# Performance work log

Measured on AMD Instinct MI355X. Metric: run time of the kernel, lower is better.

Reference implementation:

```python
import jax, jax.numpy as jnp
import numpy as np

N = 8192
D = 2048      # input_dim
DH = 1024     # input_dim // r
DO = 1024     # output_dim

def setup_inputs() -> dict:
    key = jax.random.key(0)
    ks = jax.random.split(key, 11)
    s_in = 1.0 / np.sqrt(D)
    s_h = 1.0 / np.sqrt(DH)
    return {
        "O0": jax.random.normal(ks[0], (N, D), dtype=jnp.float32),
        "Ww": jax.random.uniform(ks[1], (DH, D), jnp.float32, -s_in, s_in),
        "Wb": jax.random.uniform(ks[2], (DH,), jnp.float32, -s_in, s_in),
        "Uw": jax.random.uniform(ks[3], (DH, D), jnp.float32, -s_in, s_in),
        "Ub": jax.random.uniform(ks[4], (DH,), jnp.float32, -s_in, s_in),
        "Hw": jax.random.uniform(ks[5], (DH, D), jnp.float32, -s_in, s_in),
        "Hb": jax.random.uniform(ks[6], (DH,), jnp.float32, -s_in, s_in),
        "fc0w": jax.random.uniform(ks[7], (D, DH), jnp.float32, -s_h, s_h),
        "fc0b": jax.random.uniform(ks[8], (D,), jnp.float32, -s_h, s_h),
        "fc1w": jax.random.uniform(ks[9], (DO, D), jnp.float32, -s_in, s_in),
        "fc1b": jax.random.uniform(ks[10], (DO,), jnp.float32, -s_in, s_in),
    }

def reference(O0, Ww, Wb, Uw, Ub, Hw, Hb, fc0w, fc0b, fc1w, fc1b):
    q = O0 @ Ww.T + Wb              # [N, DH]
    k = O0 @ Uw.T + Ub              # [N, DH]
    v = O0 @ Hw.T + Hb              # [N, DH]
    scores = q @ k.T                # [N, N], unscaled as in the original
    R1 = jax.nn.softmax(scores, axis=1)
    ctx = R1 @ v                    # [N, DH]
    O1 = O0 + (ctx @ fc0w.T + fc0b) # residual, [N, D]
    O2 = O1 @ fc1w.T + fc1b         # [N, DO]
    return (O1, O2)
```

## Files before the change

kernel.cpp:

```cpp
#include <hip/hip_runtime.h>
#include <cstdint>
#include <cstddef>

typedef _Float16 f16;
typedef _Float16 f16x8 __attribute__((ext_vector_type(8)));
typedef _Float16 f16x4 __attribute__((ext_vector_type(4)));
typedef float    f32x4 __attribute__((ext_vector_type(4)));

#define BM 128
#define BN 128
#define BK 64

__global__ __launch_bounds__(256) void cvt_f32_f16(const float* __restrict__ in,
                                                   f16* __restrict__ out, int n) {
  int i = (blockIdx.x * 256 + threadIdx.x) * 4;
  if (i < n) {
    float4 v = *(const float4*)(in + i);
    f16x4 h; h[0] = (f16)v.x; h[1] = (f16)v.y; h[2] = (f16)v.z; h[3] = (f16)v.w;
    *(f16x4*)(out + i) = h;
  }
}

__global__ __launch_bounds__(256) void transpose_f16(const f16* __restrict__ in,
                                                     int ldi,
                                                     f16* __restrict__ out,
                                                     int R, int C) {
  __shared__ f16 tile[64][65];
  const int r0 = blockIdx.y * 64, c0 = blockIdx.x * 64;
  const int t = threadIdx.x;
#pragma unroll
  for (int p = 0; p < 2; p++) {
    int s = t + p * 256;
    int r = s >> 3, q = s & 7;
    f16x8 v = *(const f16x8*)(in + (size_t)(r0 + r) * ldi + c0 + q * 8);
#pragma unroll
    for (int e = 0; e < 8; e++) tile[r][q * 8 + e] = v[e];
  }
  __syncthreads();
#pragma unroll
  for (int p = 0; p < 2; p++) {
    int s = t + p * 256;
    int r = s >> 3, q = s & 7;
    f16x8 v;
#pragma unroll
    for (int e = 0; e < 8; e++) v[e] = tile[q * 8 + e][r];
    *(f16x8*)(out + (size_t)(c0 + r) * R + r0 + q * 8) = v;
  }
}

template <int MODE>
__global__ __launch_bounds__(256) void gemm_bt(
    const f16* __restrict__ A, const f16* __restrict__ B,
    int M, int N, int K, int lda, int ldb,
    const float* __restrict__ bias,
    f16* __restrict__ outH, int ldo,
    float* __restrict__ statsM, float* __restrict__ statsS, int sld,
    const float* __restrict__ alphaT,
    const float* __restrict__ resid, int ldr,
    float* __restrict__ outF, int ldof) {
  __shared__ f16 lA[BM * BK];
  __shared__ f16 lB[BN * BK];
  const int t = threadIdx.x;
  const int m0 = blockIdx.y * BM, n0 = blockIdx.x * BN;
  const int wave = t >> 6, lane = t & 63;
  const int wr = wave >> 1, wc = wave & 1;
  const int quad = lane >> 4, l16 = lane & 15;

  const int rc = lane >> 3;
  const int kcs = (lane & 7) ^ rc;
  const uint32_t offA = (uint32_t)(rc * lda + kcs * 8) * 2u;
  const uint32_t offB = (uint32_t)(rc * ldb + kcs * 8) * 2u;
  const char* bAp = (const char*)(A + (size_t)m0 * lda);
  const char* bBp = (const char*)(B + (size_t)n0 * ldb);
  const int wq = __builtin_amdgcn_readfirstlane(wave * 4);

  f32x4 acc[4][4];
#pragma unroll
  for (int i = 0; i < 4; i++)
#pragma unroll
    for (int j = 0; j < 4; j++)
#pragma unroll
      for (int e = 0; e < 4; e++) acc[i][j][e] = 0.0f;

  const int nk = K / BK;
  for (int kt = 0; kt < nk; ++kt) {
    float al[4];
    if constexpr (MODE == 2) {
      const float* ap = alphaT + (size_t)kt * M + m0 + wr * 64 + l16;
      al[0] = ap[0]; al[1] = ap[16]; al[2] = ap[32]; al[3] = ap[48];
    }
    const size_t kb = (size_t)(kt * BK) * 2;
#pragma unroll
    for (int j = 0; j < 4; j++) {
      const int c = wq + j;
      __builtin_amdgcn_global_load_lds(
          (const __attribute__((address_space(1))) void*)
              (bAp + ((size_t)(c * 8) * lda * 2 + kb) + offA),
          (__attribute__((address_space(3))) void*)(lA + c * 512), 16, 0, 0);
      __builtin_amdgcn_global_load_lds(
          (const __attribute__((address_space(1))) void*)
              (bBp + ((size_t)(c * 8) * ldb * 2 + kb) + offB),
          (__attribute__((address_space(3))) void*)(lB + c * 512), 16, 0, 0);
    }
    __syncthreads();

    f16x8 af[2][4], bf[2][4];
#pragma unroll
    for (int h = 0; h < 2; h++) {
      const int p = ((h * 4 + quad) ^ (l16 & 7)) * 8;
#pragma unroll
      for (int i = 0; i < 4; i++)
        af[h][i] = *(const f16x8*)(lA + (wr * 64 + i * 16 + l16) * 64 + p);
#pragma unroll
      for (int j = 0; j < 4; j++)
        bf[h][j] = *(const f16x8*)(lB + (wc * 64 + j * 16 + l16) * 64 + p);
    }
    if constexpr (MODE == 2) {
#pragma unroll
      for (int i = 0; i < 4; i++) {
        const f16 ah = (f16)al[i];
        af[0][i] = af[0][i] * ah;
        af[1][i] = af[1][i] * ah;
      }
    }
#pragma unroll
    for (int h = 0; h < 2; h++)
#pragma unroll
      for (int i = 0; i < 4; i++)
#pragma unroll
        for (int j = 0; j < 4; j++)
          acc[i][j] = __builtin_amdgcn_mfma_f32_16x16x32_f16(af[h][i], bf[h][j],
                                                             acc[i][j], 0, 0, 0);
    __syncthreads();
  }

  const int mrow = m0 + wr * 64;
  const int ncol = n0 + wc * 64;
  float bv[4];
  if constexpr (MODE == 0 || MODE == 3 || MODE == 4) {
#pragma unroll
    for (int j = 0; j < 4; j++) bv[j] = bias[ncol + j * 16 + l16];
  }
#pragma unroll
  for (int fi = 0; fi < 4; fi++) {
#pragma unroll
    for (int i = 0; i < 4; i++) {
      const int gr = mrow + fi * 16 + quad * 4 + i;
      if constexpr (MODE == 1) {
        float mx = fmaxf(fmaxf(acc[fi][0][i], acc[fi][1][i]),
                         fmaxf(acc[fi][2][i], acc[fi][3][i]));
        mx = fmaxf(mx, __shfl_xor(mx, 1));
        mx = fmaxf(mx, __shfl_xor(mx, 2));
        mx = fmaxf(mx, __shfl_xor(mx, 4));
        mx = fmaxf(mx, __shfl_xor(mx, 8));
        float e0 = __expf(acc[fi][0][i] - mx);
        float e1 = __expf(acc[fi][1][i] - mx);
        float e2 = __expf(acc[fi][2][i] - mx);
        float e3 = __expf(acc[fi][3][i] - mx);
        float sm = (e0 + e1) + (e2 + e3);
        sm += __shfl_xor(sm, 1);
        sm += __shfl_xor(sm, 2);
        sm += __shfl_xor(sm, 4);
        sm += __shfl_xor(sm, 8);
        if (l16 == 0) {
          statsM[(size_t)gr * sld + (blockIdx.x * 2 + wc)] = mx;
          statsS[(size_t)gr * sld + (blockIdx.x * 2 + wc)] = sm;
        }
        f16* rp = outH + (size_t)gr * ldo + ncol + l16;
        rp[0]  = (f16)e0;
        rp[16] = (f16)e1;
        rp[32] = (f16)e2;
        rp[48] = (f16)e3;
      } else if constexpr (MODE == 0) {
        f16* rp = outH + (size_t)gr * ldo + ncol + l16;
        rp[0]  = (f16)(acc[fi][0][i] + bv[0]);
        rp[16] = (f16)(acc[fi][1][i] + bv[1]);
        rp[32] = (f16)(acc[fi][2][i] + bv[2]);
        rp[48] = (f16)(acc[fi][3][i] + bv[3]);
      } else if constexpr (MODE == 2) {
        f16* rp = outH + (size_t)gr * ldo + ncol + l16;
        rp[0]  = (f16)acc[fi][0][i];
        rp[16] = (f16)acc[fi][1][i];
        rp[32] = (f16)acc[fi][2][i];
        rp[48] = (f16)acc[fi][3][i];
      } else if constexpr (MODE == 3) {
        float* rf = outF + (size_t)gr * ldof + ncol + l16;
        const float* rr = resid + (size_t)gr * ldr + ncol + l16;
        f16* rh = outH + (size_t)gr * ldo + ncol + l16;
        float o0 = acc[fi][0][i] + bv[0] + rr[0];
        float o1 = acc[fi][1][i] + bv[1] + rr[16];
        float o2 = acc[fi][2][i] + bv[2] + rr[32];
        float o3 = acc[fi][3][i] + bv[3] + rr[48];
        rf[0] = o0; rf[16] = o1; rf[32] = o2; rf[48] = o3;
        rh[0] = (f16)o0; rh[16] = (f16)o1; rh[32] = (f16)o2; rh[48] = (f16)o3;
      } else {
        float* rf = outF + (size_t)gr * ldof + ncol + l16;
        rf[0]  = acc[fi][0][i] + bv[0];
        rf[16] = acc[fi][1][i] + bv[1];
        rf[32] = acc[fi][2][i] + bv[2];
        rf[48] = acc[fi][3][i] + bv[3];
      }
    }
  }
}

__global__ __launch_bounds__(256) void alpha_from_stats(
    const float* __restrict__ sM, const float* __restrict__ sS,
    float* __restrict__ aT, int rows) {
  __shared__ float alph[128][65];
  const int t = threadIdx.x;
  const int r = t >> 2, j = t & 3;
  const int row = blockIdx.x * 64 + r;
  const float* pm = sM + (size_t)row * 128 + j * 32;
  const float* ps = sS + (size_t)row * 128 + j * 32;
  float mv[32];
  float mx = -1e30f;
#pragma unroll
  for (int c = 0; c < 32; c++) { mv[c] = pm[c]; mx = fmaxf(mx, mv[c]); }
  mx = fmaxf(mx, __shfl_xor(mx, 1));
  mx = fmaxf(mx, __shfl_xor(mx, 2));
  float ev[32];
  float sum = 0.0f;
#pragma unroll
  for (int c = 0; c < 32; c++) {
    ev[c] = __expf(mv[c] - mx);
    sum += ev[c] * ps[c];
  }
  sum += __shfl_xor(sum, 1);
  sum += __shfl_xor(sum, 2);
  const float rl = 1.0f / sum;
#pragma unroll
  for (int c = 0; c < 32; c++) alph[j * 32 + c][r] = ev[c] * rl;
  __syncthreads();
  const int wid = t >> 6, rr = t & 63;
#pragma unroll
  for (int c = 0; c < 32; c++) {
    const int tg = c * 4 + wid;
    aT[(size_t)tg * rows + blockIdx.x * 64 + rr] = alph[tg][rr];
  }
}

extern "C" void kernel_launch(void* const* d_in, const int* in_sizes, int n_in,
                              void* d_out, int out_size, void* d_ws, size_t ws_size,
                              hipStream_t stream) {
  const float* O0   = (const float*)d_in[0];
  const float* Ww   = (const float*)d_in[1];
  const float* Wb   = (const float*)d_in[2];
  const float* Uw   = (const float*)d_in[3];
  const float* Ub   = (const float*)d_in[4];
  const float* Hw   = (const float*)d_in[5];
  const float* Hb   = (const float*)d_in[6];
  const float* fc0w = (const float*)d_in[7];
  const float* fc0b = (const float*)d_in[8];
  const float* fc1w = (const float*)d_in[9];
  const float* fc1b = (const float*)d_in[10];

  const int N = 8192, D = 2048, DH = 1024, DO = 1024;
  const int NQKV = 3 * DH;

  char* w = (char*)d_ws;
  f16* Wwh   = (f16*)w; w += (size_t)DH * D * 2;
  f16* Uwh   = (f16*)w; w += (size_t)DH * D * 2;
  f16* Hwh   = (f16*)w; w += (size_t)DH * D * 2;
  f16* fc0wh = (f16*)w; w += (size_t)D * DH * 2;
  f16* fc1wh = (f16*)w; w += (size_t)DO * D * 2;
  float* aT  = (float*)w; w += (size_t)128 * N * 4;
  char* un = w; w += (size_t)N * DH * 2;
  float* statsM = (float*)un;
  float* statsS = statsM + (size_t)N * 128;
  f16* ctxh = (f16*)un;
  float* biasC = (float*)w; w += (size_t)NQKV * 4;
  w = (char*)(((uintptr_t)w + 255) & ~(uintptr_t)255);
  f16* Sb = (f16*)w;

  f16* oh   = (f16*)d_out;
  f16* qkv  = oh;
  f16* qh   = qkv;
  f16* kh   = qkv + DH;
  f16* vh   = qkv + 2 * DH;
  f16* O0h  = oh + (size_t)N * NQKV;
  f16* vT   = O0h + (size_t)N * D;
  f16* O1h  = Sb;

  {
    int n = DH * D;
    int grid = n / 1024;
    cvt_f32_f16<<<grid, 256, 0, stream>>>(Ww, Wwh, n);
    cvt_f32_f16<<<grid, 256, 0, stream>>>(Uw, Uwh, n);
    cvt_f32_f16<<<grid, 256, 0, stream>>>(Hw, Hwh, n);
    cvt_f32_f16<<<grid, 256, 0, stream>>>(fc0w, fc0wh, n);
    cvt_f32_f16<<<grid, 256, 0, stream>>>(fc1w, fc1wh, n);
    cvt_f32_f16<<<(N * D) / 1024, 256, 0, stream>>>(O0, O0h, N * D);
    hipMemcpyAsync(biasC,          Wb, DH * 4, hipMemcpyDeviceToDevice, stream);
    hipMemcpyAsync(biasC + DH,     Ub, DH * 4, hipMemcpyDeviceToDevice, stream);
    hipMemcpyAsync(biasC + 2 * DH, Hb, DH * 4, hipMemcpyDeviceToDevice, stream);
  }

  gemm_bt<0><<<dim3(NQKV / BN, N / BM), 256, 0, stream>>>(
      O0h, Wwh, N, NQKV, D, D, D, biasC,
      qkv, NQKV, nullptr, nullptr, 0, nullptr, nullptr, 0, nullptr, 0);

  transpose_f16<<<dim3(DH / 64, N / 64), 256, 0, stream>>>(vh, NQKV, vT, N, DH);

  gemm_bt<1><<<dim3(N / BN, N / BM), 256, 0, stream>>>(
      qh, kh, N, N, DH, NQKV, NQKV, nullptr, Sb, N,
      statsM, statsS, 128, nullptr, nullptr, 0, nullptr, 0);

  alpha_from_stats<<<N / 64, 256, 0, stream>>>(statsM, statsS, aT, N);

  gemm_bt<2><<<dim3(DH / BN, N / BM), 256, 0, stream>>>(
      Sb, vT, N, DH, N, N, N, nullptr, ctxh, DH,
      nullptr, nullptr, 0, aT, nullptr, 0, nullptr, 0);

  gemm_bt<3><<<dim3(D / BN, N / BM), 256, 0, stream>>>(
      ctxh, fc0wh, N, D, DH, DH, DH, fc0b, O1h, D,
      nullptr, nullptr, 0, nullptr, O0, D, (float*)d_out, D);

  gemm_bt<4><<<dim3(DO / BN, N / BM), 256, 0, stream>>>(
      O1h, fc1wh, N, DO, D, D, D, fc1b, nullptr, 0,
      nullptr, nullptr, 0, nullptr, nullptr, 0,
      (float*)d_out + (size_t)N * D, DO);
}
```

Before: 841.9 us.

## Replace 128x128 GEMM with double-buffered 256x256 ping-pong MFMA kernel

Swaps the single-buffered 128x128, 256-thread GEMM for a 256x256, 512-thread kernel. Its LDS stages are double-buffered, and global-to-LDS loads for the next k-tiles are interleaved with quarter-tile MFMA bursts. MFMA sections run at raised wave priority, and a block-index swizzle is added to improve L2 reuse. The aim is to raise arithmetic intensity and hide load latency behind compute. In exchange it uses about 130KB of LDS per block, and the narrow GEMMs (ctx and fc1) now launch only 128 workgroups, which may leave many CUs idle.

```diff
diff --git a/kernel.cpp b/kernel.cpp
--- a/kernel.cpp
+++ b/kernel.cpp
@@ -7,9 +7,7 @@
 typedef _Float16 f16x4 __attribute__((ext_vector_type(4)));
 typedef float    f32x4 __attribute__((ext_vector_type(4)));
 
-#define BM 128
-#define BN 128
-#define BK 64
+template <int V> struct IC { static constexpr int v = V; };
 
 __global__ __launch_bounds__(256) void cvt_f32_f16(const float* __restrict__ in,
                                                    f16* __restrict__ out, int n) {
@@ -49,7 +47,7 @@
 }
 
 template <int MODE>
-__global__ __launch_bounds__(256) void gemm_bt(
+__global__ __launch_bounds__(512, 2) void gemm256(
     const f16* __restrict__ A, const f16* __restrict__ B,
     int M, int N, int K, int lda, int ldb,
     const float* __restrict__ bias,
@@ -58,147 +56,233 @@
     const float* __restrict__ alphaT,
     const float* __restrict__ resid, int ldr,
     float* __restrict__ outF, int ldof) {
-  __shared__ f16 lA[BM * BK];
-  __shared__ f16 lB[BN * BK];
+  __shared__ f16 lA[2][2][128 * 64];
+  __shared__ f16 lB[2][2][128 * 64];
+  __shared__ float lAl[2][256];
+
   const int t = threadIdx.x;
-  const int m0 = blockIdx.y * BM, n0 = blockIdx.x * BN;
   const int wave = t >> 6, lane = t & 63;
-  const int wr = wave >> 1, wc = wave & 1;
+  const int wr = wave >> 2, wc = wave & 3;
   const int quad = lane >> 4, l16 = lane & 15;
-
   const int rc = lane >> 3;
   const int kcs = (lane & 7) ^ rc;
-  const uint32_t offA = (uint32_t)(rc * lda + kcs * 8) * 2u;
-  const uint32_t offB = (uint32_t)(rc * ldb + kcs * 8) * 2u;
-  const char* bAp = (const char*)(A + (size_t)m0 * lda);
-  const char* bBp = (const char*)(B + (size_t)n0 * ldb);
-  const int wq = __builtin_amdgcn_readfirstlane(wave * 4);
-
-  f32x4 acc[4][4];
-#pragma unroll
-  for (int i = 0; i < 4; i++)
-#pragma unroll
-    for (int j = 0; j < 4; j++)
-#pragma unroll
-      for (int e = 0; e < 4; e++) acc[i][j][e] = 0.0f;
-
-  const int nk = K / BK;
-  for (int kt = 0; kt < nk; ++kt) {
-    float al[4];
+
+  const int nwg = gridDim.x * gridDim.y;
+  const int bid = blockIdx.y * gridDim.x + blockIdx.x;
+  const int sb = (bid & 7) * (nwg >> 3) + (bid >> 3);
+  const int bx = sb % gridDim.x, by = sb / gridDim.x;
+  const int m0 = by * 256, n0 = bx * 256;
+  const int nk = K >> 6;
+
+  const f16* Abase = A + (size_t)m0 * lda;
+  const f16* Bbase = B + (size_t)n0 * ldb;
+
+  auto stageA = [&](int tau, int h) {
+    if (tau >= nk) return;
+    const f16* src = Abase + (size_t)(h * 128 + rc) * lda + tau * 64 + kcs * 8;
+    f16* dstu = &lA[tau & 1][h][0];
+#pragma unroll
+    for (int j = 0; j < 2; j++) {
+      const int sl = j * 8 + wave;
+      __builtin_amdgcn_global_load_lds(
+          (const __attribute__((address_space(1))) void*)(src + (size_t)sl * 8 * lda),
+          (__attribute__((address_space(3))) void*)(dstu + sl * 512), 16, 0, 0);
+    }
+  };
+  auto stageB = [&](int tau, int h) {
+    if (tau >= nk) return;
+    const f16* src = Bbase + (size_t)(h * 128 + rc) * ldb + tau * 64 + kcs * 8;
+    f16* dstu = &lB[tau & 1][h][0];
+#pragma unroll
+    for (int j = 0; j < 2; j++) {
+      const int sl = j * 8 + wave;
+      __builtin_amdgcn_global_load_lds(
+          (const __attribute__((address_space(1))) void*)(src + (size_t)sl * 8 * ldb),
+          (__attribute__((address_space(3))) void*)(dstu + sl * 512), 16, 0, 0);
+    }
+  };
+  auto stageAl = [&](int tau) {
     if constexpr (MODE == 2) {
-      const float* ap = alphaT + (size_t)kt * M + m0 + wr * 64 + l16;
-      al[0] = ap[0]; al[1] = ap[16]; al[2] = ap[32]; al[3] = ap[48];
-    }
-    const size_t kb = (size_t)(kt * BK) * 2;
-#pragma unroll
-    for (int j = 0; j < 4; j++) {
-      const int c = wq + j;
+      if (tau >= nk) return;
       __builtin_amdgcn_global_load_lds(
-          (const __attribute__((address_space(1))) void*)
-              (bAp + ((size_t)(c * 8) * lda * 2 + kb) + offA),
-          (__attribute__((address_space(3))) void*)(lA + c * 512), 16, 0, 0);
-      __builtin_amdgcn_global_load_lds(
-          (const __attribute__((address_space(1))) void*)
-              (bBp + ((size_t)(c * 8) * ldb * 2 + kb) + offB),
-          (__attribute__((address_space(3))) void*)(lB + c * 512), 16, 0, 0);
-    }
-    __syncthreads();
-
-    f16x8 af[2][4], bf[2][4];
-#pragma unroll
-    for (int h = 0; h < 2; h++) {
-      const int p = ((h * 4 + quad) ^ (l16 & 7)) * 8;
-#pragma unroll
-      for (int i = 0; i < 4; i++)
-        af[h][i] = *(const f16x8*)(lA + (wr * 64 + i * 16 + l16) * 64 + p);
-#pragma unroll
-      for (int j = 0; j < 4; j++)
-        bf[h][j] = *(const f16x8*)(lB + (wc * 64 + j * 16 + l16) * 64 + p);
-    }
-    if constexpr (MODE == 2) {
-#pragma unroll
-      for (int i = 0; i < 4; i++) {
-        const f16 ah = (f16)al[i];
-        af[0][i] = af[0][i] * ah;
-        af[1][i] = af[1][i] * ah;
+          (const __attribute__((address_space(1))) void*)(alphaT + (size_t)tau * M + m0 + lane * 4),
+          (__attribute__((address_space(3))) void*)(&lAl[tau & 1][0]), 16, 0, 0);
+    }
+  };
+
+  f32x4 acc[2][4][2][2];
+#pragma unroll
+  for (int mh = 0; mh < 2; mh++)
+#pragma unroll
+    for (int i = 0; i < 4; i++)
+#pragma unroll
+      for (int nh = 0; nh < 2; nh++)
+#pragma unroll
+        for (int j = 0; j < 2; j++)
+#pragma unroll
+          for (int e = 0; e < 4; e++) acc[mh][i][nh][j][e] = 0.0f;
+
+  f16x8 af[4][2];
+  f16x8 bf[2][2][2];
+
+  auto readA = [&](auto BUFC, auto MHC) {
+    constexpr int buf = decltype(BUFC)::v;
+    constexpr int mh = decltype(MHC)::v;
+#pragma unroll
+    for (int i = 0; i < 4; i++) {
+      const int r = i * 32 + wr * 16 + l16;
+#pragma unroll
+      for (int s = 0; s < 2; s++) {
+        const int p = ((s * 4 + quad) ^ (l16 & 7)) * 8;
+        af[i][s] = *(const f16x8*)(&lA[buf][mh][r * 64 + p]);
       }
-    }
-#pragma unroll
-    for (int h = 0; h < 2; h++)
-#pragma unroll
-      for (int i = 0; i < 4; i++)
-#pragma unroll
-        for (int j = 0; j < 4; j++)
-          acc[i][j] = __builtin_amdgcn_mfma_f32_16x16x32_f16(af[h][i], bf[h][j],
-                                                             acc[i][j], 0, 0, 0);
-    __syncthreads();
-  }
-
-  const int mrow = m0 + wr * 64;
-  const int ncol = n0 + wc * 64;
+      if constexpr (MODE == 2) {
+        const f16 ah = (f16)lAl[buf][mh * 128 + r];
+        af[i][0] = af[i][0] * ah;
+        af[i][1] = af[i][1] * ah;
+      }
+    }
+  };
+  auto readB = [&](auto BUFC, auto NHC) {
+    constexpr int buf = decltype(BUFC)::v;
+    constexpr int nh = decltype(NHC)::v;
+    const int hb = wc >> 1;
+#pragma unroll
+    for (int j = 0; j < 2; j++) {
+      const int r = (wc & 1) * 64 + nh * 32 + j * 16 + l16;
+#pragma unroll
+      for (int s = 0; s < 2; s++) {
+        const int p = ((s * 4 + quad) ^ (l16 & 7)) * 8;
+        bf[nh][j][s] = *(const f16x8*)(&lB[buf][hb][r * 64 + p]);
+      }
+    }
+  };
+  auto mfmaQ = [&](auto MHC, auto NHC) {
+    constexpr int mh = decltype(MHC)::v;
+    constexpr int nh = decltype(NHC)::v;
+    __builtin_amdgcn_s_setprio(1);
+#pragma unroll
+    for (int i = 0; i < 4; i++)
+#pragma unroll
+      for (int j = 0; j < 2; j++)
+#pragma unroll
+        for (int s = 0; s < 2; s++)
+          acc[mh][i][nh][j] = __builtin_amdgcn_mfma_f32_16x16x32_f16(
+              af[i][s], bf[nh][j][s], acc[mh][i][nh][j], 0, 0, 0);
+    __builtin_amdgcn_s_setprio(0);
+  };
+
+  auto tile4 = [&](auto BUFC, int tt, bool dr) {
+    readA(BUFC, IC<0>{});
+    readB(BUFC, IC<0>{});
+    stageA(tt + 1, 1);
+    stageAl(tt + 1);
+    __builtin_amdgcn_s_barrier();
+    asm volatile("s_waitcnt lgkmcnt(0)" ::: "memory");
+    mfmaQ(IC<0>{}, IC<0>{});
+    __builtin_amdgcn_s_barrier();
+    readB(BUFC, IC<1>{});
+    stageA(tt + 2, 0);
+    __builtin_amdgcn_s_barrier();
+    asm volatile("s_waitcnt lgkmcnt(0)" ::: "memory");
+    mfmaQ(IC<0>{}, IC<1>{});
+    __builtin_amdgcn_s_barrier();
+    readA(BUFC, IC<1>{});
+    stageB(tt + 2, 0);
+    __builtin_amdgcn_s_barrier();
+    asm volatile("s_waitcnt lgkmcnt(0)" ::: "memory");
+    mfmaQ(IC<1>{}, IC<1>{});
+    __builtin_amdgcn_s_barrier();
+    stageB(tt + 2, 1);
+    __builtin_amdgcn_s_barrier();
+    mfmaQ(IC<1>{}, IC<0>{});
+    if (dr) { asm volatile("s_waitcnt vmcnt(0)" ::: "memory"); }
+    else    { asm volatile("s_waitcnt vmcnt(6)" ::: "memory"); }
+    __builtin_amdgcn_s_barrier();
+  };
+
+  stageA(0, 0); stageB(0, 0); stageB(0, 1); stageA(0, 1);
+  stageAl(0);
+  stageA(1, 0); stageB(1, 0); stageB(1, 1);
+  asm volatile("s_waitcnt vmcnt(6)" ::: "memory");
+  __builtin_amdgcn_s_barrier();
+
+  for (int tt = 0; tt < nk; tt += 2) {
+    const bool dr = (tt + 2 >= nk);
+    tile4(IC<0>{}, tt, dr);
+    tile4(IC<1>{}, tt + 1, dr);
+  }
+
+  const int colb = n0 + wc * 64 + l16;
   float bv[4];
   if constexpr (MODE == 0 || MODE == 3 || MODE == 4) {
 #pragma unroll
-    for (int j = 0; j < 4; j++) bv[j] = bias[ncol + j * 16 + l16];
-  }
-#pragma unroll
-  for (int fi = 0; fi < 4; fi++) {
+    for (int c = 0; c < 4; c++) bv[c] = bias[colb + c * 16];
+  }
+#pragma unroll
+  for (int mh = 0; mh < 2; mh++) {
 #pragma unroll
     for (int i = 0; i < 4; i++) {
-      const int gr = mrow + fi * 16 + quad * 4 + i;
-      if constexpr (MODE == 1) {
-        float mx = fmaxf(fmaxf(acc[fi][0][i], acc[fi][1][i]),
-                         fmaxf(acc[fi][2][i], acc[fi][3][i]));
-        mx = fmaxf(mx, __shfl_xor(mx, 1));
-        mx = fmaxf(mx, __shfl_xor(mx, 2));
-        mx = fmaxf(mx, __shfl_xor(mx, 4));
-        mx = fmaxf(mx, __shfl_xor(mx, 8));
-        float e0 = __expf(acc[fi][0][i] - mx);
-        float e1 = __expf(acc[fi][1][i] - mx);
-        float e2 = __expf(acc[fi][2][i] - mx);
-        float e3 = __expf(acc[fi][3][i] - mx);
-        float sm = (e0 + e1) + (e2 + e3);
-        sm += __shfl_xor(sm, 1);
-        sm += __shfl_xor(sm, 2);
-        sm += __shfl_xor(sm, 4);
-        sm += __shfl_xor(sm, 8);
-        if (l16 == 0) {
-          statsM[(size_t)gr * sld + (blockIdx.x * 2 + wc)] = mx;
-          statsS[(size_t)gr * sld + (blockIdx.x * 2 + wc)] = sm;
+#pragma unroll
+      for (int e = 0; e < 4; e++) {
+        const int gr = m0 + mh * 128 + i * 32 + wr * 16 + quad * 4 + e;
+        const float v0 = acc[mh][i][0][0][e];
+        const float v1 = acc[mh][i][0][1][e];
+        const float v2 = acc[mh][i][1][0][e];
+        const float v3 = acc[mh][i][1][1][e];
+        if constexpr (MODE == 1) {
+          float mx = fmaxf(fmaxf(v0, v1), fmaxf(v2, v3));
+          mx = fmaxf(mx, __shfl_xor(mx, 1));
+          mx = fmaxf(mx, __shfl_xor(mx, 2));
+          mx = fmaxf(mx, __shfl_xor(mx, 4));
+          mx = fmaxf(mx, __shfl_xor(mx, 8));
+          float e0 = __expf(v0 - mx);
+          float e1 = __expf(v1 - mx);
+          float e2 = __expf(v2 - mx);
+          float e3 = __expf(v3 - mx);
+          float sm = (e0 + e1) + (e2 + e3);
+          sm += __shfl_xor(sm, 1);
+          sm += __shfl_xor(sm, 2);
+          sm += __shfl_xor(sm, 4);
+          sm += __shfl_xor(sm, 8);
+          if (l16 == 0) {
+            statsM[(size_t)gr * sld + (bx * 4 + wc)] = mx;
+            statsS[(size_t)gr * sld + (bx * 4 + wc)] = sm;
+          }
+          f16* rp = outH + (size_t)gr * ldo + colb;
+          rp[0]  = (f16)e0;
+          rp[16] = (f16)e1;
+          rp[32] = (f16)e2;
+          rp[48] = (f16)e3;
+        } else if constexpr (MODE == 0) {
+          f16* rp = outH + (size_t)gr * ldo + colb;
+          rp[0]  = (f16)(v0 + bv[0]);
+          rp[16] = (f16)(v1 + bv[1]);
+          rp[32] = (f16)(v2 + bv[2]);
+          rp[48] = (f16)(v3 + bv[3]);
+        } else if constexpr (MODE == 2) {
+          f16* rp = outH + (size_t)gr * ldo + colb;
+          rp[0]  = (f16)v0;
+          rp[16] = (f16)v1;
+          rp[32] = (f16)v2;
+          rp[48] = (f16)v3;
+        } else if constexpr (MODE == 3) {
+          float* rf = outF + (size_t)gr * ldof + colb;
+          const float* rr = resid + (size_t)gr * ldr + colb;
+          f16* rh = outH + (size_t)gr * ldo + colb;
+          float o0 = v0 + bv[0] + rr[0];
+          float o1 = v1 + bv[1] + rr[16];
+          float o2 = v2 + bv[2] + rr[32];
+          float o3 = v3 + bv[3] + rr[48];
+          rf[0] = o0; rf[16] = o1; rf[32] = o2; rf[48] = o3;
+          rh[0] = (f16)o0; rh[16] = (f16)o1; rh[32] = (f16)o2; rh[48] = (f16)o3;
+        } else {
+          float* rf = outF + (size_t)gr * ldof + colb;
+          rf[0]  = v0 + bv[0];
+          rf[16] = v1 + bv[1];
+          rf[32] = v2 + bv[2];
+          rf[48] = v3 + bv[3];
         }
-        f16* rp = outH + (size_t)gr * ldo + ncol + l16;
-        rp[0]  = (f16)e0;
-        rp[16] = (f16)e1;
-        rp[32] = (f16)e2;
-        rp[48] = (f16)e3;
-      } else if constexpr (MODE == 0) {
-        f16* rp = outH + (size_t)gr * ldo + ncol + l16;
-        rp[0]  = (f16)(acc[fi][0][i] + bv[0]);
-        rp[16] = (f16)(acc[fi][1][i] + bv[1]);
-        rp[32] = (f16)(acc[fi][2][i] + bv[2]);
-        rp[48] = (f16)(acc[fi][3][i] + bv[3]);
-      } else if constexpr (MODE == 2) {
-        f16* rp = outH + (size_t)gr * ldo + ncol + l16;
-        rp[0]  = (f16)acc[fi][0][i];
-        rp[16] = (f16)acc[fi][1][i];
-        rp[32] = (f16)acc[fi][2][i];
-        rp[48] = (f16)acc[fi][3][i];
-      } else if constexpr (MODE == 3) {
-        float* rf = outF + (size_t)gr * ldof + ncol + l16;
-        const float* rr = resid + (size_t)gr * ldr + ncol + l16;
-        f16* rh = outH + (size_t)gr * ldo + ncol + l16;
-        float o0 = acc[fi][0][i] + bv[0] + rr[0];
-        float o1 = acc[fi][1][i] + bv[1] + rr[16];
-        float o2 = acc[fi][2][i] + bv[2] + rr[32];
-        float o3 = acc[fi][3][i] + bv[3] + rr[48];
-        rf[0] = o0; rf[16] = o1; rf[32] = o2; rf[48] = o3;
-        rh[0] = (f16)o0; rh[16] = (f16)o1; rh[32] = (f16)o2; rh[48] = (f16)o3;
-      } else {
-        float* rf = outF + (size_t)gr * ldof + ncol + l16;
-        rf[0]  = acc[fi][0][i] + bv[0];
-        rf[16] = acc[fi][1][i] + bv[1];
-        rf[32] = acc[fi][2][i] + bv[2];
-        rf[48] = acc[fi][3][i] + bv[3];
       }
     }
   }
@@ -296,27 +380,27 @@
     hipMemcpyAsync(biasC + 2 * DH, Hb, DH * 4, hipMemcpyDeviceToDevice, stream);
   }
 
-  gemm_bt<0><<<dim3(NQKV / BN, N / BM), 256, 0, stream>>>(
+  gemm256<0><<<dim3(NQKV / 256, N / 256), 512, 0, stream>>>(
       O0h, Wwh, N, NQKV, D, D, D, biasC,
       qkv, NQKV, nullptr, nullptr, 0, nullptr, nullptr, 0, nullptr, 0);
 
   transpose_f16<<<dim3(DH / 64, N / 64), 256, 0, stream>>>(vh, NQKV, vT, N, DH);
 
-  gemm_bt<1><<<dim3(N / BN, N / BM), 256, 0, stream>>>(
+  gemm256<1><<<dim3(N / 256, N / 256), 512, 0, stream>>>(
       qh, kh, N, N, DH, NQKV, NQKV, nullptr, Sb, N,
       statsM, statsS, 128, nullptr, nullptr, 0, nullptr, 0);
 
   alpha_from_stats<<<N / 64, 256, 0, stream>>>(statsM, statsS, aT, N);
 
-  gemm_bt<2><<<dim3(DH / BN, N / BM), 256, 0, stream>>>(
+  gemm256<2><<<dim3(DH / 256, N / 256), 512, 0, stream>>>(
       Sb, vT, N, DH, N, N, N, nullptr, ctxh, DH,
       nullptr, nullptr, 0, aT, nullptr, 0, nullptr, 0);
 
-  gemm_bt<3><<<dim3(D / BN, N / BM), 256, 0, stream>>>(
+  gemm256<3><<<dim3(D / 256, N / 256), 512, 0, stream>>>(
       ctxh, fc0wh, N, D, DH, DH, DH, fc0b, O1h, D,
       nullptr, nullptr, 0, nullptr, O0, D, (float*)d_out, D);
 
-  gemm_bt<4><<<dim3(DO / BN, N / BM), 256, 0, stream>>>(
+  gemm256<4><<<dim3(DO / 256, N / 256), 512, 0, stream>>>(
       O1h, fc1wh, N, DO, D, D, D, fc1b, nullptr, 0,
       nullptr, nullptr, 0, nullptr, nullptr, 0,
       (float*)d_out + (size_t)N * D, DO);
```

Measured after the change: 874.8 us. +3.9%, slower.
